# Performance work log

Measured on AMD Instinct MI355X. Metric: run time of the kernel, lower is better.

## Reference

```python
import jax, jax.numpy as jnp
import numpy as np

B, L, D_MODEL, H = 2, 1920, 512, 8
DEPTH = D_MODEL // H
MAX_REL = 1921


def skew(t):
    """Huang et al. 2018 skew: pad, reshape, slice. t: (..., L, L)."""
    Lq, Lk = t.shape[-2], t.shape[-1]
    padded = jnp.pad(t, [(0, 0)] * (t.ndim - 1) + [(1, 0)])  # (..., Lq, Lk+1)
    s = padded.reshape(-1, Lk + 1, Lq)[:, 1:]                 # drop first row
    return s.reshape(t.shape)


def setup_inputs() -> dict:
    key = jax.random.key(0)
    ks = jax.random.split(key, 12)
    w = lambda k, shp: (jax.random.normal(k, shp, jnp.float32) * 0.02)
    inp = {
        "q": jax.random.normal(ks[0], (B, L, D_MODEL), jnp.float32),
        "k": jax.random.normal(ks[1], (B, L, D_MODEL), jnp.float32),
        "v": jax.random.normal(ks[2], (B, L, D_MODEL), jnp.float32),
        "mask": jnp.triu(jnp.ones((L, L), jnp.float32), k=1)[None, None],  # causal look-ahead
        "Wq": w(ks[3], (D_MODEL, D_MODEL)), "bq": jnp.zeros((D_MODEL,), jnp.float32),
        "Wk": w(ks[4], (D_MODEL, D_MODEL)), "bk": jnp.zeros((D_MODEL,), jnp.float32),
        "Wv": w(ks[5], (D_MODEL, D_MODEL)), "bv": jnp.zeros((D_MODEL,), jnp.float32),
        "E": w(ks[6], (MAX_REL, D_MODEL)),
        "Wo": w(ks[7], (D_MODEL, D_MODEL)), "bo": jnp.zeros((D_MODEL,), jnp.float32),
    }
    return inp


def reference(q, k, v, mask, Wq, bq, Wk, bk, Wv, bv, E, Wo, bo):
    Lk = k.shape[-2]
    qp = q @ Wq + bq
    kp = k @ Wk + bk
    vp = v @ Wv + bv
    # required relative embeddings (max_len >= seq_len branch): rightmost Lk rows
    e = E[MAX_REL - Lk:]                                   # (Lk, d_model)
    # split heads
    qh = qp.reshape(B, -1, H, DEPTH).transpose(0, 2, 1, 3)  # (B,H,Lq,depth)
    kh = kp.reshape(B, Lk, H, DEPTH).transpose(0, 2, 1, 3)
    vh = vp.reshape(B, Lk, H, DEPTH).transpose(0, 2, 1, 3)
    eh = e.reshape(Lk, H, DEPTH).transpose(1, 0, 2)         # (H,Lk,depth)
    QKt = jnp.einsum('bhqd,bhkd->bhqk', qh, kh)
    Srel = skew(jnp.einsum('bhqd,hkd->bhqk', qh, eh))
    logits = (QKt + Srel) / jnp.sqrt(jnp.float32(DEPTH))
    logits = logits + mask * (-1e9)
    attn = jax.nn.softmax(logits, axis=-1)                  # (B,H,Lq,Lk)
    out = jnp.einsum('bhqk,bhkd->bhqd', attn, vh)
    out = out.transpose(0, 2, 1, 3).reshape(B, -1, D_MODEL)
    out = out @ Wo + bo
    return out, attn
```

## Files before the change

kernel.cpp:

```cpp
#include <hip/hip_runtime.h>

typedef unsigned short u16;
typedef short s16x8 __attribute__((ext_vector_type(8)));
typedef float f32x4 __attribute__((ext_vector_type(4)));

#define MFMA_BF16(a, b, c) __builtin_amdgcn_mfma_f32_16x16x32_bf16((a), (b), (c), 0, 0, 0)

#define L_SEQ 1920
#define DM    512
#define NH    8
#define CH    6
#define NCHB  90

#define GLL16(gp, lp) __builtin_amdgcn_global_load_lds(                       \
    (const __attribute__((address_space(1))) void*)(gp),                      \
    (__attribute__((address_space(3))) void*)(lp), 16, 0, 0)

__device__ __forceinline__ u16 f2b(float f) {
  union { float f; unsigned u; } a; a.f = f;
  unsigned u = a.u;
  u += 0x7fffu + ((u >> 16) & 1u);
  return (u16)(u >> 16);
}
__device__ __forceinline__ float b2f(u16 h) {
  union { unsigned u; float f; } a; a.u = ((unsigned)h) << 16;
  return a.f;
}
__device__ __forceinline__ float rsum16(float x) {
  x += __shfl_xor(x, 1);
  x += __shfl_xor(x, 2);
  x += __shfl_xor(x, 4);
  x += __shfl_xor(x, 8);
  return x;
}

__global__ __launch_bounds__(256) void cvt_kernel(
    const float* __restrict__ q, const float* __restrict__ k,
    const float* __restrict__ v, const float* __restrict__ E,
    u16* __restrict__ qc, u16* __restrict__ kc,
    u16* __restrict__ vc, u16* __restrict__ Ec) {
  const float* src; u16* dst; int n;
  if (blockIdx.y == 0)      { src = q; dst = qc; n = 1966080; }
  else if (blockIdx.y == 1) { src = k; dst = kc; n = 1966080; }
  else if (blockIdx.y == 2) { src = v; dst = vc; n = 1966080; }
  else                      { src = E; dst = Ec; n = 983552; }
  const int i = (blockIdx.x * 256 + threadIdx.x) * 8;
  if (i < n) {
    float4 a = *(const float4*)(src + i);
    float4 b = *(const float4*)(src + i + 4);
    ushort4 ua; ua.x = f2b(a.x); ua.y = f2b(a.y); ua.z = f2b(a.z); ua.w = f2b(a.w);
    ushort4 ub; ub.x = f2b(b.x); ub.y = f2b(b.y); ub.z = f2b(b.z); ub.w = f2b(b.w);
    *(ushort4*)(dst + i)     = ua;
    *(ushort4*)(dst + i + 4) = ub;
  }
}

__global__ __launch_bounds__(256) void wtrans_kernel(
    const float* __restrict__ Wq, const float* __restrict__ Wk,
    const float* __restrict__ Wv, const float* __restrict__ Wo,
    u16* __restrict__ Wqt, u16* __restrict__ Wkt,
    u16* __restrict__ Wvt, u16* __restrict__ Wot) {
  const float* W; u16* Wt;
  if (blockIdx.z == 0)      { W = Wq; Wt = Wqt; }
  else if (blockIdx.z == 1) { W = Wk; Wt = Wkt; }
  else if (blockIdx.z == 2) { W = Wv; Wt = Wvt; }
  else                      { W = Wo; Wt = Wot; }
  const int k0 = blockIdx.y * 64, n0 = blockIdx.x * 64;
  __shared__ u16 T[64][72];
  const int r = threadIdx.x >> 2, c = (threadIdx.x & 3) * 16;
#pragma unroll
  for (int i = 0; i < 4; ++i) {
    float4 f = *(const float4*)(W + (size_t)(k0 + r) * 512 + n0 + c + i * 4);
    ushort4 u; u.x = f2b(f.x); u.y = f2b(f.y); u.z = f2b(f.z); u.w = f2b(f.w);
    *(ushort4*)&T[r][c + i * 4] = u;
  }
  __syncthreads();
  u16 tmp[16];
#pragma unroll
  for (int i = 0; i < 16; ++i) tmp[i] = T[c + i][r];
  u16* dst = Wt + (size_t)(n0 + r) * 512 + k0 + c;
  *(uint4*)dst       = *(uint4*)tmp;
  *(uint4*)(dst + 8) = *(uint4*)(tmp + 8);
}

__global__ __launch_bounds__(256) void vtrans_kernel(const u16* __restrict__ vp,
                                                     u16* __restrict__ vt) {
  const int bh = blockIdx.y, k0 = blockIdx.x * 64;
  const int b = bh >> 3, h = bh & 7;
  __shared__ u16 T[64][72];
  const int r = threadIdx.x >> 2, c = (threadIdx.x & 3) * 16;
  const u16* src = vp + (size_t)(b * L_SEQ + k0 + r) * DM + h * 64 + c;
  *(uint4*)&T[r][c]     = *(const uint4*)src;
  *(uint4*)&T[r][c + 8] = *(const uint4*)(src + 8);
  __syncthreads();
  u16 tmp[16];
#pragma unroll
  for (int i = 0; i < 16; ++i) tmp[i] = T[c + i][r];
  u16* dst = vt + (size_t)bh * 64 * L_SEQ + (size_t)r * L_SEQ + k0 + c;
  *(uint4*)dst       = *(uint4*)tmp;
  *(uint4*)(dst + 8) = *(uint4*)(tmp + 8);
}

template<bool OBF>
__device__ __forceinline__ void gemm512_body(const u16* Ap, const u16* Wt,
                                             const float* bias, void* Cp) {
  __shared__ u16 As[128 * 32];
  __shared__ u16 Bs[128 * 32];
  const int tid  = threadIdx.x;
  const int wv   = tid >> 6, lane = tid & 63, quad = lane >> 4, l16 = lane & 15;
  const int wr   = wv >> 1, wc = wv & 1;
  const int row0 = blockIdx.x * 128, n0 = blockIdx.y * 128;

  const int srow = tid >> 2, scol = (tid & 3) * 8;
  const u16* sA = Ap + (size_t)(row0 + srow) * 512 + scol;
  const u16* sB = Wt + (size_t)(n0  + srow) * 512 + scol;

  f32x4 acc[4][4];
#pragma unroll
  for (int i = 0; i < 4; ++i)
#pragma unroll
    for (int j = 0; j < 4; ++j) acc[i][j] = {0.f, 0.f, 0.f, 0.f};

  for (int kt = 0; kt < 16; ++kt) {
    const int k0 = kt * 32;
    GLL16(sA + k0,             &As[wv * 512]);
    GLL16(sA + k0 + 64 * 512,  &As[2048 + wv * 512]);
    GLL16(sB + k0,             &Bs[wv * 512]);
    GLL16(sB + k0 + 64 * 512,  &Bs[2048 + wv * 512]);
    __syncthreads();
    s16x8 af[4], bfr[4];
#pragma unroll
    for (int i = 0; i < 4; ++i)
      af[i]  = *(const s16x8*)&As[(wr * 64 + i * 16 + l16) * 32 + quad * 8];
#pragma unroll
    for (int i = 0; i < 4; ++i)
      bfr[i] = *(const s16x8*)&Bs[(wc * 64 + i * 16 + l16) * 32 + quad * 8];
#pragma unroll
    for (int am = 0; am < 4; ++am)
#pragma unroll
      for (int bn = 0; bn < 4; ++bn)
        acc[am][bn] = MFMA_BF16(af[am], bfr[bn], acc[am][bn]);
    __syncthreads();
  }

#pragma unroll
  for (int am = 0; am < 4; ++am)
#pragma unroll
    for (int bn = 0; bn < 4; ++bn)
#pragma unroll
      for (int r = 0; r < 4; ++r) {
        const int row = row0 + wr * 64 + am * 16 + quad * 4 + r;
        const int col = n0 + wc * 64 + bn * 16 + l16;
        float v = acc[am][bn][r] + bias[col];
        if constexpr (OBF) ((u16*)Cp)[(size_t)row * 512 + col] = f2b(v);
        else               ((float*)Cp)[(size_t)row * 512 + col] = v;
      }
}

__global__ __launch_bounds__(256) void proj3_kernel(
    const u16* __restrict__ qc, const u16* __restrict__ kc, const u16* __restrict__ vc,
    const u16* __restrict__ Wqt, const u16* __restrict__ Wkt, const u16* __restrict__ Wvt,
    const float* __restrict__ bq, const float* __restrict__ bk, const float* __restrict__ bv,
    u16* __restrict__ qp, u16* __restrict__ kp, u16* __restrict__ vp) {
  const u16* A; const u16* W; const float* bias; u16* C;
  if (blockIdx.z == 0)      { A = qc; W = Wqt; bias = bq; C = qp; }
  else if (blockIdx.z == 1) { A = kc; W = Wkt; bias = bk; C = kp; }
  else                      { A = vc; W = Wvt; bias = bv; C = vp; }
  gemm512_body<true>(A, W, bias, C);
}

__global__ __launch_bounds__(256) void outproj_kernel(
    const u16* __restrict__ A, const u16* __restrict__ Wot,
    const float* __restrict__ bo, float* __restrict__ out) {
  gemm512_body<false>(A, Wot, bo, out);
}

__global__ __launch_bounds__(256) void flash_kernel(
    const u16* __restrict__ qp, const u16* __restrict__ kp, const u16* __restrict__ vt,
    const u16* __restrict__ Ec, u16* __restrict__ phat,
    float* __restrict__ opart, float* __restrict__ spart) {
  __shared__ u16 Qs[64][72];
  __shared__ u16 Ks[64][72];
  __shared__ u16 Vs[64][72];
  __shared__ u16 Es[128][72];
  __shared__ u16 PW[4][16][136];

  const int wg  = blockIdx.x;
  const int swz = (wg & 7) * 180 + (wg >> 3);
  const int cid0 = swz % NCHB;
  const int bh   = swz / NCHB;
  const int h = bh & 7, b = bh >> 3;

  const int tid = threadIdx.x, wv = tid >> 6, lane = tid & 63;
  const int quad = lane >> 4, l16 = lane & 15;
  const int j0 = 48 - wv * 16;

  int qt = 0, c = cid0;
  for (;;) { const int n = (qt + CH) / CH; if (c < n) break; c -= n; ++qt; }
  const int kts = c * CH, kte = min(qt, kts + CH - 1);
  const int q0 = qt * 64;
  const size_t gcid = (size_t)bh * NCHB + cid0;

  const u16* qb = qp + (size_t)b * L_SEQ * DM + h * 64;
  const u16* kb = kp + (size_t)b * L_SEQ * DM + h * 64;
  const u16* vtb = vt + (size_t)bh * 64 * L_SEQ;
  const u16* Eb = Ec + h * 64;
  u16* pb = phat + ((size_t)bh * L_SEQ + q0) * L_SEQ;

  {
    const int r = tid >> 2, cc = (tid & 3) * 16;
    const u16* src = qb + (size_t)(q0 + r) * DM + cc;
    *(uint4*)&Qs[r][cc]     = *(const uint4*)src;
    *(uint4*)&Qs[r][cc + 8] = *(const uint4*)(src + 8);
  }

  float sr[4] = {0.f, 0.f, 0.f, 0.f};
  f32x4 oacc[4];
#pragma unroll
  for (int i = 0; i < 4; ++i) oacc[i] = {0.f, 0.f, 0.f, 0.f};

  for (int kt = kts; kt <= kte; ++kt) {
    const int k0 = kt * 64;
    {
      const int r = tid >> 2, cc = (tid & 3) * 16;
      const u16* src = kb + (size_t)(k0 + r) * DM + cc;
      *(uint4*)&Ks[r][cc]     = *(const uint4*)src;
      *(uint4*)&Ks[r][cc + 8] = *(const uint4*)(src + 8);
    }
    {
      const int d = tid >> 2, cc = (tid & 3) * 16;
      const u16* src = vtb + (size_t)d * L_SEQ + k0 + cc;
      *(uint4*)&Vs[d][cc]     = *(const uint4*)src;
      *(uint4*)&Vs[d][cc + 8] = *(const uint4*)(src + 8);
    }
    {
      const int j = tid >> 1, c2 = (tid & 1) * 32;
      int rg = k0 + (L_SEQ - 64) - q0 + j;
      rg = rg < 0 ? 0 : (rg > L_SEQ - 1 ? L_SEQ - 1 : rg);
      const u16* src = Eb + (size_t)(1 + rg) * DM + c2;
#pragma unroll
      for (int i = 0; i < 4; ++i)
        *(uint4*)&Es[j][c2 + i * 8] = *(const uint4*)(src + i * 8);
    }
    __syncthreads();

    f32x4 qa[4], ba[5];
#pragma unroll
    for (int i = 0; i < 4; ++i) qa[i] = {0.f, 0.f, 0.f, 0.f};
#pragma unroll
    for (int i = 0; i < 5; ++i) ba[i] = {0.f, 0.f, 0.f, 0.f};
#pragma unroll
    for (int kk = 0; kk < 2; ++kk) {
      s16x8 a = *(const s16x8*)&Qs[wv * 16 + l16][kk * 32 + quad * 8];
#pragma unroll
      for (int t = 0; t < 4; ++t) {
        s16x8 kf = *(const s16x8*)&Ks[t * 16 + l16][kk * 32 + quad * 8];
        qa[t] = MFMA_BF16(a, kf, qa[t]);
      }
#pragma unroll
      for (int u = 0; u < 5; ++u) {
        s16x8 ef = *(const s16x8*)&Es[j0 + u * 16 + l16][kk * 32 + quad * 8];
        ba[u] = MFMA_BF16(a, ef, ba[u]);
      }
    }
#pragma unroll
    for (int u = 0; u < 5; ++u)
#pragma unroll
      for (int r = 0; r < 4; ++r)
        PW[wv][quad * 4 + r][u * 16 + l16] = f2b(ba[u][r]);

    u16 pb16[4][4];
#pragma unroll
    for (int r = 0; r < 4; ++r) {
      const int lr = quad * 4 + r;
      const int qi = wv * 16 + lr;
      float ssum = 0.f;
#pragma unroll
      for (int t = 0; t < 4; ++t) {
        const float srel = b2f(PW[wv][lr][15 - lr + 16 * t + l16]);
        const float v = (qa[t][r] + srel) * 0.125f;
        const float p = ((k0 + t * 16 + l16) <= (q0 + qi)) ? __expf(v) : 0.f;
        ssum += p;
        pb16[r][t] = f2b(p);
      }
      sr[r] += rsum16(ssum);
    }
#pragma unroll
    for (int t = 0; t < 4; ++t)
#pragma unroll
      for (int r = 0; r < 4; ++r)
        PW[wv][quad * 4 + r][t * 16 + l16] = pb16[r][t];

#pragma unroll
    for (int kk = 0; kk < 2; ++kk) {
      s16x8 pa = *(const s16x8*)&PW[wv][l16][kk * 32 + quad * 8];
#pragma unroll
      for (int db = 0; db < 4; ++db) {
        s16x8 vf = *(const s16x8*)&Vs[db * 16 + l16][kk * 32 + quad * 8];
        oacc[db] = MFMA_BF16(pa, vf, oacc[db]);
      }
    }

    {
      const int prow = lane >> 3, pcol = (lane & 7) * 8;
      u16* d0 = pb + (size_t)(wv * 16 + prow) * L_SEQ + k0 + pcol;
      u16* d1 = pb + (size_t)(wv * 16 + 8 + prow) * L_SEQ + k0 + pcol;
      *(uint4*)d0 = *(const uint4*)&PW[wv][prow][pcol];
      *(uint4*)d1 = *(const uint4*)&PW[wv][8 + prow][pcol];
    }
    __syncthreads();
  }

  float* op = opart + gcid * 4096;
#pragma unroll
  for (int db = 0; db < 4; ++db)
#pragma unroll
    for (int r = 0; r < 4; ++r)
      op[(size_t)(wv * 16 + quad * 4 + r) * 64 + db * 16 + l16] = oacc[db][r];
  if (l16 == 0) {
#pragma unroll
    for (int r = 0; r < 4; ++r)
      spart[gcid * 64 + wv * 16 + quad * 4 + r] = sr[r];
  }
}

__global__ __launch_bounds__(256) void merge_kernel(
    const float* __restrict__ opart, const float* __restrict__ spart,
    u16* __restrict__ oc, float* __restrict__ sfin) {
  const int qt = blockIdx.x, bh = blockIdx.y;
  const int b = bh >> 3, h = bh & 7;
  int pre = 0;
  for (int q2 = 0; q2 < qt; ++q2) pre += (q2 + CH) / CH;
  const int nc = (qt + CH) / CH;
  const size_t gc0 = (size_t)bh * NCHB + pre;

  const int qi = threadIdx.x >> 2, ds = (threadIdx.x & 3) * 16;
  float s = 0.f;
  float4 o[4] = {{0,0,0,0},{0,0,0,0},{0,0,0,0},{0,0,0,0}};
  for (int ci = 0; ci < nc; ++ci) {
    s += spart[(gc0 + ci) * 64 + qi];
    const float* op = opart + (gc0 + ci) * 4096 + (size_t)qi * 64 + ds;
#pragma unroll
    for (int i = 0; i < 4; ++i) {
      const float4 a = *(const float4*)(op + i * 4);
      o[i].x += a.x; o[i].y += a.y; o[i].z += a.z; o[i].w += a.w;
    }
  }
  const float inv = 1.0f / s;
  u16* dst = oc + (size_t)(b * L_SEQ + qt * 64 + qi) * DM + h * 64 + ds;
#pragma unroll
  for (int i = 0; i < 4; ++i) {
    ushort4 u;
    u.x = f2b(o[i].x * inv); u.y = f2b(o[i].y * inv);
    u.z = f2b(o[i].z * inv); u.w = f2b(o[i].w * inv);
    *(ushort4*)(dst + i * 4) = u;
  }
  if ((threadIdx.x & 3) == 0) sfin[(size_t)bh * L_SEQ + qt * 64 + qi] = s;
}

__global__ __launch_bounds__(256) void fixup_kernel(
    const u16* __restrict__ phat, const float* __restrict__ sfin,
    float* __restrict__ attn) {
  const int r = blockIdx.x, bh = blockIdx.y;
  const int nlow = ((r >> 6) + 1) * 64;
  const size_t rowidx = (size_t)bh * L_SEQ + r;
  const u16* prow = phat + rowidx * L_SEQ;
  float* arow = attn + rowidx * L_SEQ;
  const int g = threadIdx.x;
  if (g >= 240) return;
  const int col = g * 8;
  float4 o0, o1;
  if (col < nlow) {
    const float fac = 1.0f / sfin[rowidx];
    uint4 u = *(const uint4*)(prow + col);
    o0.x = b2f((u16)(u.x & 0xffff)) * fac;  o0.y = b2f((u16)(u.x >> 16)) * fac;
    o0.z = b2f((u16)(u.y & 0xffff)) * fac;  o0.w = b2f((u16)(u.y >> 16)) * fac;
    o1.x = b2f((u16)(u.z & 0xffff)) * fac;  o1.y = b2f((u16)(u.z >> 16)) * fac;
    o1.z = b2f((u16)(u.w & 0xffff)) * fac;  o1.w = b2f((u16)(u.w >> 16)) * fac;
  } else {
    o0 = {0.f, 0.f, 0.f, 0.f};
    o1 = {0.f, 0.f, 0.f, 0.f};
  }
  *(float4*)(arow + col)     = o0;
  *(float4*)(arow + col + 4) = o1;
}

extern "C" void kernel_launch(void* const* d_in, const int* in_sizes, int n_in,
                              void* d_out, int out_size, void* d_ws, size_t ws_size,
                              hipStream_t stream) {
  const float* q  = (const float*)d_in[0];
  const float* k  = (const float*)d_in[1];
  const float* v  = (const float*)d_in[2];
  const float* Wq = (const float*)d_in[4];
  const float* bq = (const float*)d_in[5];
  const float* Wk = (const float*)d_in[6];
  const float* bk = (const float*)d_in[7];
  const float* Wv = (const float*)d_in[8];
  const float* bv = (const float*)d_in[9];
  const float* E  = (const float*)d_in[10];
  const float* Wo = (const float*)d_in[11];
  const float* bo = (const float*)d_in[12];

  float* out  = (float*)d_out;
  float* attn = out + (size_t)3840 * 512;

  u16* qc  = (u16*)d_ws;
  u16* kc  = qc + 1966080;
  u16* vc  = kc + 1966080;
  u16* Wqt = vc + 1966080;
  u16* Wkt = Wqt + 262144;
  u16* Wvt = Wkt + 262144;
  u16* Wot = Wvt + 262144;
  u16* Ec  = Wot + 262144;
  u16* qp  = Ec + 983552;
  u16* kp  = qp + 1966080;
  u16* vp  = kp + 1966080;
  u16* vt  = vp + 1966080;
  u16* oc  = vt + 1966080;
  u16* phat = oc + 1966080;
  float* opart = (float*)(phat + 58982400);
  float* spart = opart + (size_t)1440 * 4096;
  float* sfin  = spart + 1440 * 64;

  cvt_kernel<<<dim3(960, 4), 256, 0, stream>>>(q, k, v, E, qc, kc, vc, Ec);
  wtrans_kernel<<<dim3(8, 8, 4), 256, 0, stream>>>(Wq, Wk, Wv, Wo, Wqt, Wkt, Wvt, Wot);
  proj3_kernel<<<dim3(30, 4, 3), 256, 0, stream>>>(qc, kc, vc, Wqt, Wkt, Wvt,
                                                   bq, bk, bv, qp, kp, vp);
  vtrans_kernel<<<dim3(30, 16), 256, 0, stream>>>(vp, vt);
  flash_kernel<<<dim3(1440), 256, 0, stream>>>(qp, kp, vt, Ec, phat, opart, spart);
  merge_kernel<<<dim3(30, 16), 256, 0, stream>>>(opart, spart, oc, sfin);
  fixup_kernel<<<dim3(1920, 16), 256, 0, stream>>>(phat, sfin, attn);
  outproj_kernel<<<dim3(30, 4), 256, 0, stream>>>(oc, Wot, bo, out);
}
```

Baseline: 414.8 us.

## Load flash operands directly into registers, merge weight transpose, widen fixup rows

```diff
diff --git a/kernel.cpp b/kernel.cpp
--- a/kernel.cpp
+++ b/kernel.cpp
@@ -38,7 +38,39 @@
     const float* __restrict__ q, const float* __restrict__ k,
     const float* __restrict__ v, const float* __restrict__ E,
     u16* __restrict__ qc, u16* __restrict__ kc,
-    u16* __restrict__ vc, u16* __restrict__ Ec) {
+    u16* __restrict__ vc, u16* __restrict__ Ec,
+    const float* __restrict__ Wq, const float* __restrict__ Wk,
+    const float* __restrict__ Wv, const float* __restrict__ Wo,
+    u16* __restrict__ Wqt, u16* __restrict__ Wkt,
+    u16* __restrict__ Wvt, u16* __restrict__ Wot) {
+  __shared__ u16 T[64][72];
+  if (blockIdx.y == 4) {
+    const int bx = blockIdx.x;
+    if (bx >= 256) return;
+    const float* W; u16* Wt;
+    const int z = bx >> 6;
+    if (z == 0)      { W = Wq; Wt = Wqt; }
+    else if (z == 1) { W = Wk; Wt = Wkt; }
+    else if (z == 2) { W = Wv; Wt = Wvt; }
+    else             { W = Wo; Wt = Wot; }
+    const int rem = bx & 63;
+    const int k0 = (rem >> 3) * 64, n0 = (rem & 7) * 64;
+    const int r = threadIdx.x >> 2, c = (threadIdx.x & 3) * 16;
+#pragma unroll
+    for (int i = 0; i < 4; ++i) {
+      float4 f = *(const float4*)(W + (size_t)(k0 + r) * 512 + n0 + c + i * 4);
+      ushort4 u; u.x = f2b(f.x); u.y = f2b(f.y); u.z = f2b(f.z); u.w = f2b(f.w);
+      *(ushort4*)&T[r][c + i * 4] = u;
+    }
+    __syncthreads();
+    u16 tmp[16];
+#pragma unroll
+    for (int i = 0; i < 16; ++i) tmp[i] = T[c + i][r];
+    u16* dst = Wt + (size_t)(n0 + r) * 512 + k0 + c;
+    *(uint4*)dst       = *(uint4*)tmp;
+    *(uint4*)(dst + 8) = *(uint4*)(tmp + 8);
+    return;
+  }
   const float* src; u16* dst; int n;
   if (blockIdx.y == 0)      { src = q; dst = qc; n = 1966080; }
   else if (blockIdx.y == 1) { src = k; dst = kc; n = 1966080; }
@@ -55,34 +87,6 @@
   }
 }
 
-__global__ __launch_bounds__(256) void wtrans_kernel(
-    const float* __restrict__ Wq, const float* __restrict__ Wk,
-    const float* __restrict__ Wv, const float* __restrict__ Wo,
-    u16* __restrict__ Wqt, u16* __restrict__ Wkt,
-    u16* __restrict__ Wvt, u16* __restrict__ Wot) {
-  const float* W; u16* Wt;
-  if (blockIdx.z == 0)      { W = Wq; Wt = Wqt; }
-  else if (blockIdx.z == 1) { W = Wk; Wt = Wkt; }
-  else if (blockIdx.z == 2) { W = Wv; Wt = Wvt; }
-  else                      { W = Wo; Wt = Wot; }
-  const int k0 = blockIdx.y * 64, n0 = blockIdx.x * 64;
-  __shared__ u16 T[64][72];
-  const int r = threadIdx.x >> 2, c = (threadIdx.x & 3) * 16;
-#pragma unroll
-  for (int i = 0; i < 4; ++i) {
-    float4 f = *(const float4*)(W + (size_t)(k0 + r) * 512 + n0 + c + i * 4);
-    ushort4 u; u.x = f2b(f.x); u.y = f2b(f.y); u.z = f2b(f.z); u.w = f2b(f.w);
-    *(ushort4*)&T[r][c + i * 4] = u;
-  }
-  __syncthreads();
-  u16 tmp[16];
-#pragma unroll
-  for (int i = 0; i < 16; ++i) tmp[i] = T[c + i][r];
-  u16* dst = Wt + (size_t)(n0 + r) * 512 + k0 + c;
-  *(uint4*)dst       = *(uint4*)tmp;
-  *(uint4*)(dst + 8) = *(uint4*)(tmp + 8);
-}
-
 __global__ __launch_bounds__(256) void vtrans_kernel(const u16* __restrict__ vp,
                                                      u16* __restrict__ vt) {
   const int bh = blockIdx.y, k0 = blockIdx.x * 64;
@@ -179,10 +183,6 @@
     const u16* __restrict__ qp, const u16* __restrict__ kp, const u16* __restrict__ vt,
     const u16* __restrict__ Ec, u16* __restrict__ phat,
     float* __restrict__ opart, float* __restrict__ spart) {
-  __shared__ u16 Qs[64][72];
-  __shared__ u16 Ks[64][72];
-  __shared__ u16 Vs[64][72];
-  __shared__ u16 Es[128][72];
   __shared__ u16 PW[4][16][136];
 
   const int wg  = blockIdx.x;
@@ -207,11 +207,11 @@
   const u16* Eb = Ec + h * 64;
   u16* pb = phat + ((size_t)bh * L_SEQ + q0) * L_SEQ;
 
+  s16x8 qf[2];
   {
-    const int r = tid >> 2, cc = (tid & 3) * 16;
-    const u16* src = qb + (size_t)(q0 + r) * DM + cc;
-    *(uint4*)&Qs[r][cc]     = *(const uint4*)src;
-    *(uint4*)&Qs[r][cc + 8] = *(const uint4*)(src + 8);
+    const u16* src = qb + (size_t)(q0 + wv * 16 + l16) * DM + quad * 8;
+    qf[0] = *(const s16x8*)src;
+    qf[1] = *(const s16x8*)(src + 32);
   }
 
   float sr[4] = {0.f, 0.f, 0.f, 0.f};
@@ -221,28 +221,6 @@
 
   for (int kt = kts; kt <= kte; ++kt) {
     const int k0 = kt * 64;
-    {
-      const int r = tid >> 2, cc = (tid & 3) * 16;
-      const u16* src = kb + (size_t)(k0 + r) * DM + cc;
-      *(uint4*)&Ks[r][cc]     = *(const uint4*)src;
-      *(uint4*)&Ks[r][cc + 8] = *(const uint4*)(src + 8);
-    }
-    {
-      const int d = tid >> 2, cc = (tid & 3) * 16;
-      const u16* src = vtb + (size_t)d * L_SEQ + k0 + cc;
-      *(uint4*)&Vs[d][cc]     = *(const uint4*)src;
-      *(uint4*)&Vs[d][cc + 8] = *(const uint4*)(src + 8);
-    }
-    {
-      const int j = tid >> 1, c2 = (tid & 1) * 32;
-      int rg = k0 + (L_SEQ - 64) - q0 + j;
-      rg = rg < 0 ? 0 : (rg > L_SEQ - 1 ? L_SEQ - 1 : rg);
-      const u16* src = Eb + (size_t)(1 + rg) * DM + c2;
-#pragma unroll
-      for (int i = 0; i < 4; ++i)
-        *(uint4*)&Es[j][c2 + i * 8] = *(const uint4*)(src + i * 8);
-    }
-    __syncthreads();
 
     f32x4 qa[4], ba[5];
 #pragma unroll
@@ -251,18 +229,24 @@
     for (int i = 0; i < 5; ++i) ba[i] = {0.f, 0.f, 0.f, 0.f};
 #pragma unroll
     for (int kk = 0; kk < 2; ++kk) {
-      s16x8 a = *(const s16x8*)&Qs[wv * 16 + l16][kk * 32 + quad * 8];
-#pragma unroll
-      for (int t = 0; t < 4; ++t) {
-        s16x8 kf = *(const s16x8*)&Ks[t * 16 + l16][kk * 32 + quad * 8];
-        qa[t] = MFMA_BF16(a, kf, qa[t]);
+      s16x8 kf[4], ef[5];
+#pragma unroll
+      for (int t = 0; t < 4; ++t)
+        kf[t] = *(const s16x8*)(kb + (size_t)(k0 + t * 16 + l16) * DM + kk * 32 + quad * 8);
+#pragma unroll
+      for (int u = 0; u < 5; ++u) {
+        int rg = k0 + (L_SEQ - 64) - q0 + j0 + u * 16 + l16;
+        rg = rg < 0 ? 0 : (rg > L_SEQ - 1 ? L_SEQ - 1 : rg);
+        ef[u] = *(const s16x8*)(Eb + (size_t)(1 + rg) * DM + kk * 32 + quad * 8);
       }
-#pragma unroll
-      for (int u = 0; u < 5; ++u) {
-        s16x8 ef = *(const s16x8*)&Es[j0 + u * 16 + l16][kk * 32 + quad * 8];
-        ba[u] = MFMA_BF16(a, ef, ba[u]);
-      }
-    }
+      __builtin_amdgcn_s_setprio(1);
+#pragma unroll
+      for (int t = 0; t < 4; ++t) qa[t] = MFMA_BF16(qf[kk], kf[t], qa[t]);
+#pragma unroll
+      for (int u = 0; u < 5; ++u) ba[u] = MFMA_BF16(qf[kk], ef[u], ba[u]);
+      __builtin_amdgcn_s_setprio(0);
+    }
+
 #pragma unroll
     for (int u = 0; u < 5; ++u)
 #pragma unroll
@@ -294,11 +278,13 @@
 #pragma unroll
     for (int kk = 0; kk < 2; ++kk) {
       s16x8 pa = *(const s16x8*)&PW[wv][l16][kk * 32 + quad * 8];
+      __builtin_amdgcn_s_setprio(1);
 #pragma unroll
       for (int db = 0; db < 4; ++db) {
-        s16x8 vf = *(const s16x8*)&Vs[db * 16 + l16][kk * 32 + quad * 8];
+        s16x8 vf = *(const s16x8*)(vtb + (size_t)(db * 16 + l16) * L_SEQ + k0 + kk * 32 + quad * 8);
         oacc[db] = MFMA_BF16(pa, vf, oacc[db]);
       }
+      __builtin_amdgcn_s_setprio(0);
     }
 
     {
@@ -308,7 +294,6 @@
       *(uint4*)d0 = *(const uint4*)&PW[wv][prow][pcol];
       *(uint4*)d1 = *(const uint4*)&PW[wv][8 + prow][pcol];
     }
-    __syncthreads();
   }
 
   float* op = opart + gcid * 4096;
@@ -361,28 +346,27 @@
 __global__ __launch_bounds__(256) void fixup_kernel(
     const u16* __restrict__ phat, const float* __restrict__ sfin,
     float* __restrict__ attn) {
-  const int r = blockIdx.x, bh = blockIdx.y;
+  const int bh = blockIdx.y;
+  const int r  = blockIdx.x * 8 + (threadIdx.x >> 5);
+  const int lc = threadIdx.x & 31;
   const int nlow = ((r >> 6) + 1) * 64;
   const size_t rowidx = (size_t)bh * L_SEQ + r;
   const u16* prow = phat + rowidx * L_SEQ;
   float* arow = attn + rowidx * L_SEQ;
-  const int g = threadIdx.x;
-  if (g >= 240) return;
-  const int col = g * 8;
-  float4 o0, o1;
-  if (col < nlow) {
-    const float fac = 1.0f / sfin[rowidx];
-    uint4 u = *(const uint4*)(prow + col);
-    o0.x = b2f((u16)(u.x & 0xffff)) * fac;  o0.y = b2f((u16)(u.x >> 16)) * fac;
-    o0.z = b2f((u16)(u.y & 0xffff)) * fac;  o0.w = b2f((u16)(u.y >> 16)) * fac;
-    o1.x = b2f((u16)(u.z & 0xffff)) * fac;  o1.y = b2f((u16)(u.z >> 16)) * fac;
-    o1.z = b2f((u16)(u.w & 0xffff)) * fac;  o1.w = b2f((u16)(u.w >> 16)) * fac;
-  } else {
-    o0 = {0.f, 0.f, 0.f, 0.f};
-    o1 = {0.f, 0.f, 0.f, 0.f};
-  }
-  *(float4*)(arow + col)     = o0;
-  *(float4*)(arow + col + 4) = o1;
+  const float fac = 1.0f / sfin[rowidx];
+#pragma unroll
+  for (int j = 0; j < 15; ++j) {
+    const int col = (lc + j * 32) * 4;
+    float4 o;
+    if (col < nlow) {
+      uint2 u = *(const uint2*)(prow + col);
+      o.x = b2f((u16)(u.x & 0xffff)) * fac;  o.y = b2f((u16)(u.x >> 16)) * fac;
+      o.z = b2f((u16)(u.y & 0xffff)) * fac;  o.w = b2f((u16)(u.y >> 16)) * fac;
+    } else {
+      o = {0.f, 0.f, 0.f, 0.f};
+    }
+    *(float4*)(arow + col) = o;
+  }
 }
 
 extern "C" void kernel_launch(void* const* d_in, const int* in_sizes, int n_in,
@@ -422,13 +406,13 @@
   float* spart = opart + (size_t)1440 * 4096;
   float* sfin  = spart + 1440 * 64;
 
-  cvt_kernel<<<dim3(960, 4), 256, 0, stream>>>(q, k, v, E, qc, kc, vc, Ec);
-  wtrans_kernel<<<dim3(8, 8, 4), 256, 0, stream>>>(Wq, Wk, Wv, Wo, Wqt, Wkt, Wvt, Wot);
+  cvt_kernel<<<dim3(960, 5), 256, 0, stream>>>(q, k, v, E, qc, kc, vc, Ec,
+                                               Wq, Wk, Wv, Wo, Wqt, Wkt, Wvt, Wot);
   proj3_kernel<<<dim3(30, 4, 3), 256, 0, stream>>>(qc, kc, vc, Wqt, Wkt, Wvt,
                                                    bq, bk, bv, qp, kp, vp);
   vtrans_kernel<<<dim3(30, 16), 256, 0, stream>>>(vp, vt);
   flash_kernel<<<dim3(1440), 256, 0, stream>>>(qp, kp, vt, Ec, phat, opart, spart);
   merge_kernel<<<dim3(30, 16), 256, 0, stream>>>(opart, spart, oc, sfin);
-  fixup_kernel<<<dim3(1920, 16), 256, 0, stream>>>(phat, sfin, attn);
+  fixup_kernel<<<dim3(240, 16), 256, 0, stream>>>(phat, sfin, attn);
   outproj_kernel<<<dim3(30, 4), 256, 0, stream>>>(oc, Wot, bo, out);
 }
```

Result: slower. 468.4 us (+12.9%).
